# Kernel tuning notes

Hardware: AMD Instinct MI355X
Metric: run time of the kernel (lower is better)

## Reference

```python
import jax, jax.numpy as jnp
import numpy as np

L, D, H, EXP = 6, 512, 8, 4
DH = D // H
EPS = 1e-3  # keras LayerNormalization default epsilon


def _layer_norm(x, gamma, beta):
    mu = jnp.mean(x, axis=-1, keepdims=True)
    var = jnp.mean(jnp.square(x - mu), axis=-1, keepdims=True)
    return (x - mu) * jax.lax.rsqrt(var + EPS) * gamma + beta


def setup_inputs() -> dict:
    key = jax.random.key(0)
    ks = jax.random.split(key, 10)
    B, S = 8, 1024
    s_attn = 1.0 / np.sqrt(D)
    s_ffn1 = 1.0 / np.sqrt(D)
    s_ffn2 = 1.0 / np.sqrt(D * EXP)
    return {
        "x": jax.random.normal(ks[0], (B, S, D), dtype=jnp.float32),
        "Wq": jax.random.normal(ks[1], (L, D, D), dtype=jnp.float32) * s_attn,
        "Wk": jax.random.normal(ks[2], (L, D, D), dtype=jnp.float32) * s_attn,
        "Wv": jax.random.normal(ks[3], (L, D, D), dtype=jnp.float32) * s_attn,
        "Wo": jax.random.normal(ks[4], (L, D, D), dtype=jnp.float32) * s_attn,
        "W1": jax.random.normal(ks[5], (L, D, D * EXP), dtype=jnp.float32) * s_ffn1,
        "b1": jnp.zeros((L, D * EXP), dtype=jnp.float32),
        "W2": jax.random.normal(ks[6], (L, D * EXP, D), dtype=jnp.float32) * s_ffn2,
        "b2": jnp.zeros((L, D), dtype=jnp.float32),
        "g_attn": jnp.ones((L, D), dtype=jnp.float32),
        "be_attn": jnp.zeros((L, D), dtype=jnp.float32),
        "g_ffn": jnp.ones((L, D), dtype=jnp.float32),
        "be_ffn": jnp.zeros((L, D), dtype=jnp.float32),
    }


def _self_attention(y, wq, wk, wv, wo):
    B, S, _ = y.shape
    q = (y @ wq).reshape(B, S, H, DH)
    k = (y @ wk).reshape(B, S, H, DH)
    v = (y @ wv).reshape(B, S, H, DH)
    scores = jnp.einsum("bqhd,bkhd->bhqk", q, k) / np.sqrt(float(DH))
    attn = jax.nn.softmax(scores, axis=-1)
    z = jnp.einsum("bhqk,bkhd->bqhd", attn, v).reshape(B, S, D)
    return z @ wo


def reference(x, Wq, Wk, Wv, Wo, W1, b1, W2, b2, g_attn, be_attn, g_ffn, be_ffn):
    encoded = x
    for l in range(L):
        # pre-LN self-attention + residual (dropout=identity at inference)
        attended = _layer_norm(encoded, g_attn[l], be_attn[l])
        attended = _self_attention(attended, Wq[l], Wk[l], Wv[l], Wo[l])
        attended = encoded + attended
        # pre-LN FFN + residual
        h = _layer_norm(attended, g_ffn[l], be_ffn[l])
        h = jax.nn.relu(h @ W1[l] + b1[l]) @ W2[l] + b2[l]
        encoded = attended + h
    return encoded
```

## Files before the change

### kernel.cpp

```cpp
#include <hip/hip_runtime.h>


#define SEQ 1024
#define ROWS 8192
#define QKVW 1536

using bf16x8 = __attribute__((ext_vector_type(8))) short;
using f32x4  = __attribute__((ext_vector_type(4))) float;

__device__ __forceinline__ unsigned short f2bf(float f) {
  union { float f; unsigned u; } v; v.f = f;
  unsigned r = v.u + 0x7FFFu + ((v.u >> 16) & 1u);
  return (unsigned short)(r >> 16);
}
__device__ __forceinline__ float bf2f(unsigned short b) {
  union { unsigned u; float f; } v; v.u = ((unsigned)b) << 16;
  return v.f;
}

__device__ __forceinline__ float exp2_fast(float x) {
  float r;
  asm("v_exp_f32 %0, %1" : "=v"(r) : "v"(x));
  return r;
}

__device__ __forceinline__ unsigned cvtpk_bf16(float a, float b) {
  unsigned r;
  asm("v_cvt_pk_bf16_f32 %0, %1, %2" : "=v"(r) : "v"(a), "v"(b));
  return r;
}

__device__ __forceinline__ void gl16(const void* g, void* l) {
  typedef const unsigned int __attribute__((address_space(1)))* GP;
  typedef unsigned int __attribute__((address_space(3)))* LP;
  __builtin_amdgcn_global_load_lds((GP)g, (LP)l, 16, 0, 0);
}

__global__ __launch_bounds__(256) void transpose_cast_k(
    const float* __restrict__ W, unsigned short* __restrict__ Wt,
    int K, int N, int lstride, float scale)
{
  __shared__ float tile[32][33];
  const int l = blockIdx.z;
  const float* Wl = W + (size_t)l * K * N;
  unsigned short* Wtl = Wt + (size_t)l * lstride;
  const int k0 = blockIdx.y * 32, n0 = blockIdx.x * 32;
  const int tx = threadIdx.x & 31, ty = threadIdx.x >> 5;
  #pragma unroll
  for (int i = ty; i < 32; i += 8)
    tile[i][tx] = Wl[(size_t)(k0 + i) * N + n0 + tx];
  __syncthreads();
  #pragma unroll
  for (int i = ty; i < 32; i += 8)
    Wtl[(size_t)(n0 + i) * K + k0 + tx] = f2bf(tile[tx][i] * scale);
}

__global__ __launch_bounds__(256) void wprep4_k(
    const float* __restrict__ Wq, const float* __restrict__ Wk,
    const float* __restrict__ Wv, const float* __restrict__ Wo,
    unsigned short* __restrict__ WtQKV, unsigned short* __restrict__ WtO,
    float qscale)
{
  __shared__ float tile[32][33];
  const int z = blockIdx.z, l = z >> 2, which = z & 3;
  const float* W;
  unsigned short* Wtl;
  float scale = 1.0f;
  switch (which) {
    case 0: W = Wq; Wtl = WtQKV + (size_t)l * QKVW * 512;          scale = qscale; break;
    case 1: W = Wk; Wtl = WtQKV + (size_t)l * QKVW * 512 + 262144; break;
    case 2: W = Wv; Wtl = WtQKV + (size_t)l * QKVW * 512 + 524288; break;
    default: W = Wo; Wtl = WtO + (size_t)l * 262144;               break;
  }
  const float* Wl = W + (size_t)l * 512 * 512;
  const int k0 = blockIdx.y * 32, n0 = blockIdx.x * 32;
  const int tx = threadIdx.x & 31, ty = threadIdx.x >> 5;
  #pragma unroll
  for (int i = ty; i < 32; i += 8)
    tile[i][tx] = Wl[(size_t)(k0 + i) * 512 + n0 + tx];
  __syncthreads();
  #pragma unroll
  for (int i = ty; i < 32; i += 8)
    Wtl[(size_t)(n0 + i) * 512 + k0 + tx] = f2bf(tile[tx][i] * scale);
}

__global__ __launch_bounds__(256) void cvt_k(
    const float* __restrict__ x, unsigned short* __restrict__ y, int n8)
{
  const int i = blockIdx.x * 256 + threadIdx.x;
  if (i >= n8) return;
  const float4 a = reinterpret_cast<const float4*>(x)[i * 2];
  const float4 b = reinterpret_cast<const float4*>(x)[i * 2 + 1];
  uint4 o;
  o.x = (unsigned)f2bf(a.x) | ((unsigned)f2bf(a.y) << 16);
  o.y = (unsigned)f2bf(a.z) | ((unsigned)f2bf(a.w) << 16);
  o.z = (unsigned)f2bf(b.x) | ((unsigned)f2bf(b.y) << 16);
  o.w = (unsigned)f2bf(b.z) | ((unsigned)f2bf(b.w) << 16);
  reinterpret_cast<uint4*>(y)[i] = o;
}

__global__ __launch_bounds__(256) void ln_k(
    const unsigned short* __restrict__ x, const float* __restrict__ g,
    const float* __restrict__ be, unsigned short* __restrict__ y, int rows)
{
  const int wid = (blockIdx.x << 2) | (threadIdx.x >> 6);
  const int lane = threadIdx.x & 63;
  if (wid >= rows) return;
  const uint4 u = reinterpret_cast<const uint4*>(x + (size_t)wid * 512)[lane];
  float f[8];
  f[0] = bf2f((unsigned short)(u.x & 0xffffu)); f[1] = bf2f((unsigned short)(u.x >> 16));
  f[2] = bf2f((unsigned short)(u.y & 0xffffu)); f[3] = bf2f((unsigned short)(u.y >> 16));
  f[4] = bf2f((unsigned short)(u.z & 0xffffu)); f[5] = bf2f((unsigned short)(u.z >> 16));
  f[6] = bf2f((unsigned short)(u.w & 0xffffu)); f[7] = bf2f((unsigned short)(u.w >> 16));
  float s = (f[0] + f[1] + f[2] + f[3]) + (f[4] + f[5] + f[6] + f[7]);
  #pragma unroll
  for (int m = 32; m >= 1; m >>= 1) s += __shfl_xor(s, m);
  const float mu = s * (1.0f / 512.0f);
  float d[8], q = 0.0f;
  #pragma unroll
  for (int j = 0; j < 8; j++) { d[j] = f[j] - mu; q += d[j] * d[j]; }
  #pragma unroll
  for (int m = 32; m >= 1; m >>= 1) q += __shfl_xor(q, m);
  const float inv = rsqrtf(q * (1.0f / 512.0f) + 1e-3f);
  const float4 g0 = reinterpret_cast<const float4*>(g)[lane * 2];
  const float4 g1 = reinterpret_cast<const float4*>(g)[lane * 2 + 1];
  const float4 h0 = reinterpret_cast<const float4*>(be)[lane * 2];
  const float4 h1 = reinterpret_cast<const float4*>(be)[lane * 2 + 1];
  uint4 o;
  o.x = (unsigned)f2bf(d[0] * inv * g0.x + h0.x) | ((unsigned)f2bf(d[1] * inv * g0.y + h0.y) << 16);
  o.y = (unsigned)f2bf(d[2] * inv * g0.z + h0.z) | ((unsigned)f2bf(d[3] * inv * g0.w + h0.w) << 16);
  o.z = (unsigned)f2bf(d[4] * inv * g1.x + h1.x) | ((unsigned)f2bf(d[5] * inv * g1.y + h1.y) << 16);
  o.w = (unsigned)f2bf(d[6] * inv * g1.z + h1.z) | ((unsigned)f2bf(d[7] * inv * g1.w + h1.w) << 16);
  reinterpret_cast<uint4*>(y + (size_t)wid * 512)[lane] = o;
}

template<bool RELU, bool HASBIAS, bool HASRES, bool OUTBF, bool QKV>
__global__ __launch_bounds__(256) void gemm128_k(
    const unsigned short* __restrict__ A,
    const unsigned short* __restrict__ Wt,
    const float* __restrict__ bias,
    const float* __restrict__ res,
    void* __restrict__ outp, unsigned short* __restrict__ vt,
    int M, int N, int K)
{
  __shared__ __align__(16) unsigned short As0[4096], Bs0[4096];
  __shared__ __align__(16) unsigned short As1[4096], Bs1[4096];
  const int t = threadIdx.x;
  const int nwg = gridDim.x * gridDim.y;
  const int bid = blockIdx.y * gridDim.x + blockIdx.x;
  const int nid = (bid & 7) * (nwg >> 3) + (bid >> 3);
  const int bx = nid % gridDim.x, by = nid / gridDim.x;
  const int m0 = by * 128, n0 = bx * 128;
  const int w = t >> 6, lane = t & 63, llo = lane & 15, lhi = lane >> 4;
  const int wr = w >> 1, wc = w & 1;

  const int sr = t >> 2, sg = (t & 3) ^ ((t >> 3) & 3);
  const unsigned short* pa = &A[(size_t)(m0 + sr) * K + sg * 8];
  const unsigned short* pb = &Wt[(size_t)(n0 + sr) * K + sg * 8];

#define GSTAGE128(AsX, BsX, koff) do { \
    gl16(pa + (koff), &AsX[t * 8]); \
    gl16(pa + (size_t)64 * K + (koff), &AsX[2048 + t * 8]); \
    gl16(pb + (koff), &BsX[t * 8]); \
    gl16(pb + (size_t)64 * K + (koff), &BsX[2048 + t * 8]); \
  } while (0)

  const int pgo = (lhi ^ ((llo >> 1) & 3)) * 8;

#define GCOMP128(AsX, BsX) do { \
    bf16x8 af[4], bfr[4]; \
    _Pragma("unroll") \
    for (int f = 0; f < 4; f++) { \
      af[f]  = *reinterpret_cast<const bf16x8*>(&AsX[(wr * 64 + f * 16 + llo) * 32 + pgo]); \
      bfr[f] = *reinterpret_cast<const bf16x8*>(&BsX[(wc * 64 + f * 16 + llo) * 32 + pgo]); \
    } \
    _Pragma("unroll") \
    for (int fi = 0; fi < 4; fi++) \
      _Pragma("unroll") \
      for (int fj = 0; fj < 4; fj++) \
        acc[fi][fj] = __builtin_amdgcn_mfma_f32_16x16x32_bf16(af[fi], bfr[fj], acc[fi][fj], 0, 0, 0); \
  } while (0)

  f32x4 acc[4][4] = {};
  GSTAGE128(As0, Bs0, 0);
  for (int k0 = 0; k0 < K; k0 += 64) {
    __syncthreads();
    GSTAGE128(As1, Bs1, k0 + 32);
    GCOMP128(As0, Bs0);
    __syncthreads();
    if (k0 + 64 < K) GSTAGE128(As0, Bs0, k0 + 64);
    GCOMP128(As1, Bs1);
  }
#undef GSTAGE128
#undef GCOMP128

  if (QKV && n0 >= 1024) {
    const int bb2 = by >> 3;
    const int s0 = (by & 7) * 128;
    const int bh = bb2 * 8 + ((bx - 8) << 1) + wc;
    #pragma unroll
    for (int fi = 0; fi < 4; fi++)
      #pragma unroll
      for (int fj = 0; fj < 4; fj++) {
        ushort4 o;
        o.x = f2bf(acc[fi][fj][0]);
        o.y = f2bf(acc[fi][fj][1]);
        o.z = f2bf(acc[fi][fj][2]);
        o.w = f2bf(acc[fi][fj][3]);
        const int dv = fj * 16 + llo;
        *reinterpret_cast<ushort4*>(
            &vt[((size_t)bh * 64 + dv) * SEQ + s0 + wr * 64 + fi * 16 + lhi * 4]) = o;
      }
    return;
  }

  const int row0 = m0 + wr * 64, col0 = n0 + wc * 64;
  #pragma unroll
  for (int fi = 0; fi < 4; fi++)
    #pragma unroll
    for (int fj = 0; fj < 4; fj++)
      #pragma unroll
      for (int i = 0; i < 4; i++) {
        const int row = row0 + fi * 16 + lhi * 4 + i;
        const int col = col0 + fj * 16 + llo;
        float v = acc[fi][fj][i];
        if (HASBIAS) v += bias[col];
        if (HASRES)  v += res[(size_t)row * N + col];
        if (RELU)    v = fmaxf(v, 0.0f);
        if (OUTBF) ((unsigned short*)outp)[(size_t)row * N + col] = f2bf(v);
        else       ((float*)outp)[(size_t)row * N + col] = v;
      }
}

template<bool RELU, bool HASBIAS, bool HASRES, bool OUTBF, bool RESBF>
__global__ __launch_bounds__(256) void gemm64_k(
    const unsigned short* __restrict__ A,
    const unsigned short* __restrict__ Wt,
    const float* __restrict__ bias,
    const void* __restrict__ res,
    void* __restrict__ outp, int M, int N, int K)
{
  __shared__ __align__(16) unsigned short As0[2048], Bs0[4096];
  __shared__ __align__(16) unsigned short As1[2048], Bs1[4096];
  const int t = threadIdx.x;
  const int nwg = gridDim.x * gridDim.y;
  const int bid = blockIdx.y * gridDim.x + blockIdx.x;
  const int nid = (bid & 7) * (nwg >> 3) + (bid >> 3);
  const int bx = nid % gridDim.x, by = nid / gridDim.x;
  const int m0 = by * 64, n0 = bx * 128;
  const int w = t >> 6, lane = t & 63, llo = lane & 15, lhi = lane >> 4;
  const int wr = w >> 1, wc = w & 1;

  const int sr = t >> 2, sg = (t & 3) ^ ((t >> 3) & 3);
  const unsigned short* pa = &A[(size_t)(m0 + sr) * K + sg * 8];
  const unsigned short* pb = &Wt[(size_t)(n0 + sr) * K + sg * 8];

#define GSTAGE64(AsX, BsX, koff) do { \
    gl16(pa + (koff), &AsX[t * 8]); \
    gl16(pb + (koff), &BsX[t * 8]); \
    gl16(pb + (size_t)64 * K + (koff), &BsX[2048 + t * 8]); \
  } while (0)

  const int pgo = (lhi ^ ((llo >> 1) & 3)) * 8;

#define GCOMP64(AsX, BsX) do { \
    bf16x8 af[2], bfr[4]; \
    _Pragma("unroll") \
    for (int f = 0; f < 2; f++) \
      af[f] = *reinterpret_cast<const bf16x8*>(&AsX[(wr * 32 + f * 16 + llo) * 32 + pgo]); \
    _Pragma("unroll") \
    for (int f = 0; f < 4; f++) \
      bfr[f] = *reinterpret_cast<const bf16x8*>(&BsX[(wc * 64 + f * 16 + llo) * 32 + pgo]); \
    _Pragma("unroll") \
    for (int fi = 0; fi < 2; fi++) \
      _Pragma("unroll") \
      for (int fj = 0; fj < 4; fj++) \
        acc[fi][fj] = __builtin_amdgcn_mfma_f32_16x16x32_bf16(af[fi], bfr[fj], acc[fi][fj], 0, 0, 0); \
  } while (0)

  f32x4 acc[2][4] = {};
  GSTAGE64(As0, Bs0, 0);
  for (int k0 = 0; k0 < K; k0 += 64) {
    __syncthreads();
    GSTAGE64(As1, Bs1, k0 + 32);
    GCOMP64(As0, Bs0);
    __syncthreads();
    if (k0 + 64 < K) GSTAGE64(As0, Bs0, k0 + 64);
    GCOMP64(As1, Bs1);
  }
#undef GSTAGE64
#undef GCOMP64

  const int row0 = m0 + wr * 32, col0 = n0 + wc * 64;
  #pragma unroll
  for (int fi = 0; fi < 2; fi++)
    #pragma unroll
    for (int fj = 0; fj < 4; fj++)
      #pragma unroll
      for (int i = 0; i < 4; i++) {
        const int row = row0 + fi * 16 + lhi * 4 + i;
        const int col = col0 + fj * 16 + llo;
        float v = acc[fi][fj][i];
        if (HASBIAS) v += bias[col];
        if (HASRES) {
          if (RESBF) v += bf2f(((const unsigned short*)res)[(size_t)row * N + col]);
          else       v += ((const float*)res)[(size_t)row * N + col];
        }
        if (RELU)    v = fmaxf(v, 0.0f);
        if (OUTBF) ((unsigned short*)outp)[(size_t)row * N + col] = f2bf(v);
        else       ((float*)outp)[(size_t)row * N + col] = v;
      }
}

__global__ __launch_bounds__(256) void attn_k(
    const unsigned short* __restrict__ QKV,
    const unsigned short* __restrict__ VT,
    unsigned short* __restrict__ Zb)
{
  __shared__ __align__(16) unsigned short Ks0[4096], Vs0[4096];
  __shared__ __align__(16) unsigned short Ks1[4096], Vs1[4096];
  __shared__ __align__(16) unsigned short Ps[8192];

  const int t = threadIdx.x;
  const int h = blockIdx.x, qt = blockIdx.y, bb = blockIdx.z;
  const int w = t >> 6, lane = t & 63, llo = lane & 15, lhi = lane >> 4;
  const size_t rowb = (size_t)bb * SEQ;
  const int kcol = 512 + h * 64;
  const size_t vtb = (size_t)(bb * 8 + h) * 64 * SEQ;

  bf16x8 aq[2][2];
  #pragma unroll
  for (int mi = 0; mi < 2; mi++)
    #pragma unroll
    for (int ds = 0; ds < 2; ds++)
      aq[mi][ds] = *reinterpret_cast<const bf16x8*>(
          &QKV[(rowb + qt * 128 + w * 32 + mi * 16 + llo) * QKVW + h * 64 + ds * 32 + lhi * 8]);

  const int cA = t, cB = 256 + t;
  const int gA = cA >> 6, lA = cA & 63, gB = cB >> 6, lB = cB & 63;
  const unsigned short* kpA = &QKV[(rowb + (gA >> 1) * 16 + (lA & 15)) * QKVW + kcol + (gA & 1) * 32 + (lA >> 4) * 8];
  const unsigned short* kpB = &QKV[(rowb + (gB >> 1) * 16 + (lB & 15)) * QKVW + kcol + (gB & 1) * 32 + (lB >> 4) * 8];
  const unsigned short* vpA = &VT[vtb + (size_t)((gA >> 1) * 16 + (lA & 15)) * SEQ + (gA & 1) * 32 + (lA >> 4) * 8];
  const unsigned short* vpB = &VT[vtb + (size_t)((gB >> 1) * 16 + (lB & 15)) * SEQ + (gB & 1) * 32 + (lB >> 4) * 8];

#define ASTAGE(KsX, VsX, ktt) do { \
    gl16(kpA + (size_t)(ktt) * 64 * QKVW, &KsX[cA * 8]); \
    gl16(kpB + (size_t)(ktt) * 64 * QKVW, &KsX[cB * 8]); \
    gl16(vpA + (ktt) * 64, &VsX[cA * 8]); \
    gl16(vpB + (ktt) * 64, &VsX[cB * 8]); \
  } while (0)

  const int psw = w * 2048;
  const int lsw = llo & 7;

#define ACOMP(KsX, VsX) do { \
    f32x4 s_[2][4]; \
    _Pragma("unroll") \
    for (int mi = 0; mi < 2; mi++) \
      _Pragma("unroll") \
      for (int fj = 0; fj < 4; fj++) \
        _Pragma("unroll") \
        for (int i = 0; i < 4; i++) s_[mi][fj][i] = -16.0f; \
    _Pragma("unroll") \
    for (int ds = 0; ds < 2; ds++) \
      _Pragma("unroll") \
      for (int fj = 0; fj < 4; fj++) { \
        bf16x8 bk = *reinterpret_cast<const bf16x8*>(&KsX[((fj * 2 + ds) * 64 + lane) * 8]); \
        s_[0][fj] = __builtin_amdgcn_mfma_f32_16x16x32_bf16(bk, aq[0][ds], s_[0][fj], 0, 0, 0); \
        s_[1][fj] = __builtin_amdgcn_mfma_f32_16x16x32_bf16(bk, aq[1][ds], s_[1][fj], 0, 0, 0); \
      } \
    _Pragma("unroll") \
    for (int mi = 0; mi < 2; mi++) \
      _Pragma("unroll") \
      for (int fj = 0; fj < 4; fj++) { \
        const float p0 = exp2_fast(s_[mi][fj][0]); \
        const float p1 = exp2_fast(s_[mi][fj][1]); \
        const float p2 = exp2_fast(s_[mi][fj][2]); \
        const float p3 = exp2_fast(s_[mi][fj][3]); \
        l_[mi] += (p0 + p1) + (p2 + p3); \
        uint2 uv; uv.x = cvtpk_bf16(p0, p1); uv.y = cvtpk_bf16(p2, p3); \
        const int pg = ((fj << 1) | (lhi >> 1)) ^ lsw; \
        *reinterpret_cast<uint2*>(&Ps[psw + (mi * 16 + llo) * 64 + pg * 8 + (lhi & 1) * 4]) = uv; \
      } \
    _Pragma("unroll") \
    for (int ks = 0; ks < 2; ks++) { \
      const int prg = (((ks << 2) | lhi) ^ lsw) << 3; \
      bf16x8 ap0 = *reinterpret_cast<const bf16x8*>(&Ps[psw + llo * 64 + prg]); \
      bf16x8 ap1 = *reinterpret_cast<const bf16x8*>(&Ps[psw + (16 + llo) * 64 + prg]); \
      _Pragma("unroll") \
      for (int fo = 0; fo < 4; fo++) { \
        bf16x8 bv = *reinterpret_cast<const bf16x8*>(&VsX[((fo * 2 + ks) * 64 + lane) * 8]); \
        o_[0][fo] = __builtin_amdgcn_mfma_f32_16x16x32_bf16(ap0, bv, o_[0][fo], 0, 0, 0); \
        o_[1][fo] = __builtin_amdgcn_mfma_f32_16x16x32_bf16(ap1, bv, o_[1][fo], 0, 0, 0); \
      } \
    } \
  } while (0)

  float l_[2] = {0.0f, 0.0f};
  f32x4 o_[2][4] = {};

  ASTAGE(Ks0, Vs0, 0);
  for (int kt = 0; kt < 16; kt += 2) {
    __syncthreads();
    ASTAGE(Ks1, Vs1, kt + 1);
    ACOMP(Ks0, Vs0);
    __syncthreads();
    if (kt + 2 < 16) ASTAGE(Ks0, Vs0, kt + 2);
    ACOMP(Ks1, Vs1);
  }
#undef ASTAGE
#undef ACOMP

  #pragma unroll
  for (int mi = 0; mi < 2; mi++) {
    l_[mi] += __shfl_xor(l_[mi], 16);
    l_[mi] += __shfl_xor(l_[mi], 32);
    l_[mi] = 1.0f / l_[mi];
  }

  #pragma unroll
  for (int mi = 0; mi < 2; mi++)
    #pragma unroll
    for (int i = 0; i < 4; i++) {
      const float li = __shfl(l_[mi], lhi * 4 + i);
      #pragma unroll
      for (int fo = 0; fo < 4; fo++) {
        const float v = o_[mi][fo][i] * li;
        Zb[(rowb + qt * 128 + w * 32 + mi * 16 + lhi * 4 + i) * 512 + h * 64 + fo * 16 + llo] = f2bf(v);
      }
    }
}

extern "C" void kernel_launch(void* const* d_in, const int* in_sizes, int n_in,
                              void* d_out, int out_size, void* d_ws, size_t ws_size,
                              hipStream_t stream)
{
  const float* x   = (const float*)d_in[0];
  const float* Wq  = (const float*)d_in[1];
  const float* Wk  = (const float*)d_in[2];
  const float* Wv  = (const float*)d_in[3];
  const float* Wo  = (const float*)d_in[4];
  const float* W1  = (const float*)d_in[5];
  const float* b1  = (const float*)d_in[6];
  const float* W2  = (const float*)d_in[7];
  const float* b2  = (const float*)d_in[8];
  const float* ga  = (const float*)d_in[9];
  const float* ba  = (const float*)d_in[10];
  const float* gf  = (const float*)d_in[11];
  const float* bfn = (const float*)d_in[12];
  float* out = (float*)d_out;

  char* p = (char*)d_ws;
  auto alloc = [&](size_t bytes) { void* r = (void*)p; p += (bytes + 255) & ~(size_t)255; return r; };
  unsigned short* E0 = (unsigned short*)alloc((size_t)ROWS * 512 * 2);
  unsigned short* E1 = (unsigned short*)alloc((size_t)ROWS * 512 * 2);
  unsigned short* Ybf   = (unsigned short*)alloc((size_t)ROWS * 512 * 2);
  unsigned short* QKVbf = (unsigned short*)alloc((size_t)ROWS * QKVW * 2);
  unsigned short* H1bf  = (unsigned short*)alloc((size_t)ROWS * 2048 * 2);
  unsigned short* VT    = H1bf;
  unsigned short* WtQKV = (unsigned short*)alloc(6ull * QKVW * 512 * 2);
  unsigned short* WtO   = (unsigned short*)alloc(6ull * 512 * 512 * 2);
  unsigned short* Wt1   = (unsigned short*)alloc(6ull * 2048 * 512 * 2);
  unsigned short* Wt2   = (unsigned short*)alloc(6ull * 512 * 2048 * 2);
  unsigned short* Zbf   = Ybf;

  const float qscale = 0.125f * 1.44269504f;
  wprep4_k<<<dim3(16, 16, 24), 256, 0, stream>>>(Wq, Wk, Wv, Wo, WtQKV, WtO, qscale);
  transpose_cast_k<<<dim3(64, 16, 6), 256, 0, stream>>>(W1, Wt1, 512, 2048, 1048576, 1.0f);
  transpose_cast_k<<<dim3(16, 64, 6), 256, 0, stream>>>(W2, Wt2, 2048, 512, 1048576, 1.0f);
  cvt_k<<<2048, 256, 0, stream>>>(x, E0, ROWS * 512 / 8);

  for (int l = 0; l < 6; l++) {
    ln_k<<<2048, 256, 0, stream>>>(E0, ga + l * 512, ba + l * 512, Ybf, ROWS);
    gemm128_k<false, false, false, true, true><<<dim3(12, 64), 256, 0, stream>>>(
        Ybf, WtQKV + (size_t)l * QKVW * 512, nullptr, nullptr, QKVbf, VT, ROWS, QKVW, 512);
    attn_k<<<dim3(8, 8, 8), 256, 0, stream>>>(QKVbf, VT, Zbf);
    gemm64_k<false, false, true, true, true><<<dim3(4, 128), 256, 0, stream>>>(
        Zbf, WtO + (size_t)l * 262144, nullptr, E0, E1, ROWS, 512, 512);
    ln_k<<<2048, 256, 0, stream>>>(E1, gf + l * 512, bfn + l * 512, Ybf, ROWS);
    gemm64_k<true, true, false, true, false><<<dim3(16, 128), 256, 0, stream>>>(
        Ybf, Wt1 + (size_t)l * 1048576, b1 + l * 2048, nullptr, H1bf, ROWS, 2048, 512);
    if (l < 5)
      gemm64_k<false, true, true, true, true><<<dim3(4, 128), 256, 0, stream>>>(
          H1bf, Wt2 + (size_t)l * 1048576, b2 + l * 512, E1, E0, ROWS, 512, 2048);
    else
      gemm64_k<false, true, true, false, true><<<dim3(4, 128), 256, 0, stream>>>(
          H1bf, Wt2 + (size_t)l * 1048576, b2 + l * 512, E1, out, ROWS, 512, 2048);
  }
}
```

Baseline: 818.6 us.

## Fold LayerNorm into GEMM epilogues via gamma-scaled weights and stats

LayerNorm is rewritten algebraically: gamma is folded into the transposed QKV and W1 weights, and per-column correction vectors (sum of gamma*W and beta*W plus bias) are precomputed. A light stat kernel now writes only per-row mean and inverse std, and the GEMM epilogue applies inv*(acc - mu*C1) + C2. This removes the normalized-activation write and read per LayerNorm. The FFN1 GEMM also moves from the 64-row to the 128-row tile kernel. The risk is numerical: the bf16 GEMM now runs on un-centered inputs and variance is computed as E[x^2]-mu^2.

```diff
diff --git a/kernel.cpp b/kernel.cpp
--- a/kernel.cpp
+++ b/kernel.cpp
@@ -58,6 +58,7 @@
 __global__ __launch_bounds__(256) void wprep4_k(
     const float* __restrict__ Wq, const float* __restrict__ Wk,
     const float* __restrict__ Wv, const float* __restrict__ Wo,
+    const float* __restrict__ ga,
     unsigned short* __restrict__ WtQKV, unsigned short* __restrict__ WtO,
     float qscale)
 {
@@ -79,9 +80,57 @@
   for (int i = ty; i < 32; i += 8)
     tile[i][tx] = Wl[(size_t)(k0 + i) * 512 + n0 + tx];
   __syncthreads();
+  const float gv = (which < 3) ? ga[l * 512 + k0 + tx] * scale : 1.0f;
   #pragma unroll
   for (int i = ty; i < 32; i += 8)
-    Wtl[(size_t)(n0 + i) * 512 + k0 + tx] = f2bf(tile[tx][i] * scale);
+    Wtl[(size_t)(n0 + i) * 512 + k0 + tx] = f2bf(tile[tx][i] * gv);
+}
+
+__global__ __launch_bounds__(256) void wprep1_k(
+    const float* __restrict__ W, const float* __restrict__ gf,
+    unsigned short* __restrict__ Wt)
+{
+  __shared__ float tile[32][33];
+  const int l = blockIdx.z;
+  const float* Wl = W + (size_t)l * 512 * 2048;
+  unsigned short* Wtl = Wt + (size_t)l * 1048576;
+  const int k0 = blockIdx.y * 32, n0 = blockIdx.x * 32;
+  const int tx = threadIdx.x & 31, ty = threadIdx.x >> 5;
+  #pragma unroll
+  for (int i = ty; i < 32; i += 8)
+    tile[i][tx] = Wl[(size_t)(k0 + i) * 2048 + n0 + tx];
+  __syncthreads();
+  const float gv = gf[l * 512 + k0 + tx];
+  #pragma unroll
+  for (int i = ty; i < 32; i += 8)
+    Wtl[(size_t)(n0 + i) * 512 + k0 + tx] = f2bf(tile[tx][i] * gv);
+}
+
+__global__ __launch_bounds__(256) void cvec_k(
+    const float* __restrict__ W, const float* __restrict__ g,
+    const float* __restrict__ be, const float* __restrict__ bias, float scale,
+    float* __restrict__ C1, float* __restrict__ C2, int N, int Cstride)
+{
+  const int l = blockIdx.y;
+  const float* Wl = W + (size_t)l * 512 * N;
+  const int t = threadIdx.x;
+  const int n = blockIdx.x * 64 + (t & 63);
+  const int sl = t >> 6;
+  float s1 = 0.0f, s2 = 0.0f;
+  for (int k = sl * 128; k < sl * 128 + 128; k++) {
+    const float w = Wl[(size_t)k * N + n];
+    s1 += g[l * 512 + k] * w;
+    s2 += be[l * 512 + k] * w;
+  }
+  __shared__ float r1[256], r2[256];
+  r1[t] = s1; r2[t] = s2;
+  __syncthreads();
+  if (sl == 0) {
+    s1 = r1[t] + r1[t + 64] + r1[t + 128] + r1[t + 192];
+    s2 = r2[t] + r2[t + 64] + r2[t + 128] + r2[t + 192];
+    C1[(size_t)l * Cstride + n] = s1 * scale;
+    C2[(size_t)l * Cstride + n] = s2 * scale + (bias ? bias[(size_t)l * N + n] : 0.0f);
+  }
 }
 
 __global__ __launch_bounds__(256) void cvt_k(
@@ -99,9 +148,8 @@
   reinterpret_cast<uint4*>(y)[i] = o;
 }
 
-__global__ __launch_bounds__(256) void ln_k(
-    const unsigned short* __restrict__ x, const float* __restrict__ g,
-    const float* __restrict__ be, unsigned short* __restrict__ y, int rows)
+__global__ __launch_bounds__(256) void stat_k(
+    const unsigned short* __restrict__ x, float2* __restrict__ mui, int rows)
 {
   const int wid = (blockIdx.x << 2) | (threadIdx.x >> 6);
   const int lane = threadIdx.x & 63;
@@ -112,34 +160,27 @@
   f[2] = bf2f((unsigned short)(u.y & 0xffffu)); f[3] = bf2f((unsigned short)(u.y >> 16));
   f[4] = bf2f((unsigned short)(u.z & 0xffffu)); f[5] = bf2f((unsigned short)(u.z >> 16));
   f[6] = bf2f((unsigned short)(u.w & 0xffffu)); f[7] = bf2f((unsigned short)(u.w >> 16));
-  float s = (f[0] + f[1] + f[2] + f[3]) + (f[4] + f[5] + f[6] + f[7]);
-  #pragma unroll
-  for (int m = 32; m >= 1; m >>= 1) s += __shfl_xor(s, m);
-  const float mu = s * (1.0f / 512.0f);
-  float d[8], q = 0.0f;
-  #pragma unroll
-  for (int j = 0; j < 8; j++) { d[j] = f[j] - mu; q += d[j] * d[j]; }
-  #pragma unroll
-  for (int m = 32; m >= 1; m >>= 1) q += __shfl_xor(q, m);
-  const float inv = rsqrtf(q * (1.0f / 512.0f) + 1e-3f);
-  const float4 g0 = reinterpret_cast<const float4*>(g)[lane * 2];
-  const float4 g1 = reinterpret_cast<const float4*>(g)[lane * 2 + 1];
-  const float4 h0 = reinterpret_cast<const float4*>(be)[lane * 2];
-  const float4 h1 = reinterpret_cast<const float4*>(be)[lane * 2 + 1];
-  uint4 o;
-  o.x = (unsigned)f2bf(d[0] * inv * g0.x + h0.x) | ((unsigned)f2bf(d[1] * inv * g0.y + h0.y) << 16);
-  o.y = (unsigned)f2bf(d[2] * inv * g0.z + h0.z) | ((unsigned)f2bf(d[3] * inv * g0.w + h0.w) << 16);
-  o.z = (unsigned)f2bf(d[4] * inv * g1.x + h1.x) | ((unsigned)f2bf(d[5] * inv * g1.y + h1.y) << 16);
-  o.w = (unsigned)f2bf(d[6] * inv * g1.z + h1.z) | ((unsigned)f2bf(d[7] * inv * g1.w + h1.w) << 16);
-  reinterpret_cast<uint4*>(y + (size_t)wid * 512)[lane] = o;
-}
-
-template<bool RELU, bool HASBIAS, bool HASRES, bool OUTBF, bool QKV>
+  float s = 0.0f, q = 0.0f;
+  #pragma unroll
+  for (int j = 0; j < 8; j++) { s += f[j]; q += f[j] * f[j]; }
+  #pragma unroll
+  for (int m = 32; m >= 1; m >>= 1) { s += __shfl_xor(s, m); q += __shfl_xor(q, m); }
+  if (lane == 0) {
+    const float mu = s * (1.0f / 512.0f);
+    const float inv = rsqrtf(q * (1.0f / 512.0f) - mu * mu + 1e-3f);
+    mui[wid] = make_float2(mu, inv);
+  }
+}
+
+template<bool RELU, bool HASBIAS, bool HASRES, bool OUTBF, bool QKV, bool LNF>
 __global__ __launch_bounds__(256) void gemm128_k(
     const unsigned short* __restrict__ A,
     const unsigned short* __restrict__ Wt,
     const float* __restrict__ bias,
     const float* __restrict__ res,
+    const float2* __restrict__ MUI,
+    const float* __restrict__ C1,
+    const float* __restrict__ C2,
     void* __restrict__ outp, unsigned short* __restrict__ vt,
     int M, int N, int K)
 {
@@ -194,6 +235,23 @@
 #undef GSTAGE128
 #undef GCOMP128
 
+  const int row0 = m0 + wr * 64, col0 = n0 + wc * 64;
+
+  float2 muiA[4][4];
+  float c1v[4], c2v[4];
+  if (LNF) {
+    #pragma unroll
+    for (int fi = 0; fi < 4; fi++)
+      #pragma unroll
+      for (int i = 0; i < 4; i++)
+        muiA[fi][i] = MUI[row0 + fi * 16 + lhi * 4 + i];
+    #pragma unroll
+    for (int fj = 0; fj < 4; fj++) {
+      c1v[fj] = C1[col0 + fj * 16 + llo];
+      c2v[fj] = C2[col0 + fj * 16 + llo];
+    }
+  }
+
   if (QKV && n0 >= 1024) {
     const int bb2 = by >> 3;
     const int s0 = (by & 7) * 128;
@@ -202,11 +260,15 @@
     for (int fi = 0; fi < 4; fi++)
       #pragma unroll
       for (int fj = 0; fj < 4; fj++) {
+        float vv[4];
+        #pragma unroll
+        for (int i = 0; i < 4; i++) {
+          float v = acc[fi][fj][i];
+          if (LNF) v = muiA[fi][i].y * (v - muiA[fi][i].x * c1v[fj]) + c2v[fj];
+          vv[i] = v;
+        }
         ushort4 o;
-        o.x = f2bf(acc[fi][fj][0]);
-        o.y = f2bf(acc[fi][fj][1]);
-        o.z = f2bf(acc[fi][fj][2]);
-        o.w = f2bf(acc[fi][fj][3]);
+        o.x = f2bf(vv[0]); o.y = f2bf(vv[1]); o.z = f2bf(vv[2]); o.w = f2bf(vv[3]);
         const int dv = fj * 16 + llo;
         *reinterpret_cast<ushort4*>(
             &vt[((size_t)bh * 64 + dv) * SEQ + s0 + wr * 64 + fi * 16 + lhi * 4]) = o;
@@ -214,7 +276,6 @@
     return;
   }
 
-  const int row0 = m0 + wr * 64, col0 = n0 + wc * 64;
   #pragma unroll
   for (int fi = 0; fi < 4; fi++)
     #pragma unroll
@@ -224,6 +285,7 @@
         const int row = row0 + fi * 16 + lhi * 4 + i;
         const int col = col0 + fj * 16 + llo;
         float v = acc[fi][fj][i];
+        if (LNF)     v = muiA[fi][i].y * (v - muiA[fi][i].x * c1v[fj]) + c2v[fj];
         if (HASBIAS) v += bias[col];
         if (HASRES)  v += res[(size_t)row * N + col];
         if (RELU)    v = fmaxf(v, 0.0f);
@@ -454,7 +516,7 @@
   auto alloc = [&](size_t bytes) { void* r = (void*)p; p += (bytes + 255) & ~(size_t)255; return r; };
   unsigned short* E0 = (unsigned short*)alloc((size_t)ROWS * 512 * 2);
   unsigned short* E1 = (unsigned short*)alloc((size_t)ROWS * 512 * 2);
-  unsigned short* Ybf   = (unsigned short*)alloc((size_t)ROWS * 512 * 2);
+  unsigned short* Zbf   = (unsigned short*)alloc((size_t)ROWS * 512 * 2);
   unsigned short* QKVbf = (unsigned short*)alloc((size_t)ROWS * QKVW * 2);
   unsigned short* H1bf  = (unsigned short*)alloc((size_t)ROWS * 2048 * 2);
   unsigned short* VT    = H1bf;
@@ -462,24 +524,37 @@
   unsigned short* WtO   = (unsigned short*)alloc(6ull * 512 * 512 * 2);
   unsigned short* Wt1   = (unsigned short*)alloc(6ull * 2048 * 512 * 2);
   unsigned short* Wt2   = (unsigned short*)alloc(6ull * 512 * 2048 * 2);
-  unsigned short* Zbf   = Ybf;
+  float2* MUI0 = (float2*)alloc((size_t)ROWS * 8);
+  float2* MUI1 = (float2*)alloc((size_t)ROWS * 8);
+  float* C1qkv = (float*)alloc(6ull * QKVW * 4);
+  float* C2qkv = (float*)alloc(6ull * QKVW * 4);
+  float* C1f   = (float*)alloc(6ull * 2048 * 4);
+  float* C2f   = (float*)alloc(6ull * 2048 * 4);
 
   const float qscale = 0.125f * 1.44269504f;
-  wprep4_k<<<dim3(16, 16, 24), 256, 0, stream>>>(Wq, Wk, Wv, Wo, WtQKV, WtO, qscale);
-  transpose_cast_k<<<dim3(64, 16, 6), 256, 0, stream>>>(W1, Wt1, 512, 2048, 1048576, 1.0f);
+  wprep4_k<<<dim3(16, 16, 24), 256, 0, stream>>>(Wq, Wk, Wv, Wo, ga, WtQKV, WtO, qscale);
+  wprep1_k<<<dim3(64, 16, 6), 256, 0, stream>>>(W1, gf, Wt1);
   transpose_cast_k<<<dim3(16, 64, 6), 256, 0, stream>>>(W2, Wt2, 2048, 512, 1048576, 1.0f);
+  cvec_k<<<dim3(8, 6), 256, 0, stream>>>(Wq, ga, ba, nullptr, qscale, C1qkv,        C2qkv,        512, QKVW);
+  cvec_k<<<dim3(8, 6), 256, 0, stream>>>(Wk, ga, ba, nullptr, 1.0f,   C1qkv + 512,  C2qkv + 512,  512, QKVW);
+  cvec_k<<<dim3(8, 6), 256, 0, stream>>>(Wv, ga, ba, nullptr, 1.0f,   C1qkv + 1024, C2qkv + 1024, 512, QKVW);
+  cvec_k<<<dim3(32, 6), 256, 0, stream>>>(W1, gf, bfn, b1,    1.0f,   C1f,          C2f,          2048, 2048);
   cvt_k<<<2048, 256, 0, stream>>>(x, E0, ROWS * 512 / 8);
 
   for (int l = 0; l < 6; l++) {
-    ln_k<<<2048, 256, 0, stream>>>(E0, ga + l * 512, ba + l * 512, Ybf, ROWS);
-    gemm128_k<false, false, false, true, true><<<dim3(12, 64), 256, 0, stream>>>(
-        Ybf, WtQKV + (size_t)l * QKVW * 512, nullptr, nullptr, QKVbf, VT, ROWS, QKVW, 512);
+    stat_k<<<2048, 256, 0, stream>>>(E0, MUI0, ROWS);
+    gemm128_k<false, false, false, true, true, true><<<dim3(12, 64), 256, 0, stream>>>(
+        E0, WtQKV + (size_t)l * QKVW * 512, nullptr, nullptr,
+        MUI0, C1qkv + (size_t)l * QKVW, C2qkv + (size_t)l * QKVW,
+        QKVbf, VT, ROWS, QKVW, 512);
     attn_k<<<dim3(8, 8, 8), 256, 0, stream>>>(QKVbf, VT, Zbf);
     gemm64_k<false, false, true, true, true><<<dim3(4, 128), 256, 0, stream>>>(
         Zbf, WtO + (size_t)l * 262144, nullptr, E0, E1, ROWS, 512, 512);
-    ln_k<<<2048, 256, 0, stream>>>(E1, gf + l * 512, bfn + l * 512, Ybf, ROWS);
-    gemm64_k<true, true, false, true, false><<<dim3(16, 128), 256, 0, stream>>>(
-        Ybf, Wt1 + (size_t)l * 1048576, b1 + l * 2048, nullptr, H1bf, ROWS, 2048, 512);
+    stat_k<<<2048, 256, 0, stream>>>(E1, MUI1, ROWS);
+    gemm128_k<true, false, false, true, false, true><<<dim3(16, 64), 256, 0, stream>>>(
+        E1, Wt1 + (size_t)l * 1048576, nullptr, nullptr,
+        MUI1, C1f + (size_t)l * 2048, C2f + (size_t)l * 2048,
+        H1bf, nullptr, ROWS, 2048, 512);
     if (l < 5)
       gemm64_k<false, true, true, true, true><<<dim3(4, 128), 256, 0, stream>>>(
           H1bf, Wt2 + (size_t)l * 1048576, b2 + l * 512, E1, E0, ROWS, 512, 2048);
```

New measurement: 929.9 us. 1.14x slower.
